# Kernel tuning notes

Measured on AMD Instinct MI355X. Metric: run time of the kernel, lower is better.

## Reference

```python
import jax, jax.numpy as jnp
import numpy as np

# Perfect 8-ary tree, 6 levels, level-order node indexing.
K = 8            # children per internal node
D = 512          # embedding_dim
P = 8            # number of dependency types (num_params)
OFF = [0, 1, 9, 73, 585, 4681, 37449]  # level start offsets; N = 37449
N = OFF[-1]


def setup_inputs() -> dict:
    key = jax.random.key(0)
    ks = jax.random.split(key, 8)
    s = 1.0 / np.sqrt(D)  # torch default-ish init scale, avoids LSTM saturation
    return {
        "embeddings": jax.random.normal(ks[0], (N, D), dtype=jnp.float32),
        "dep_types": jax.random.randint(ks[1], (N,), 0, P, dtype=jnp.int32),
        "W_dep": jax.random.normal(ks[2], (P, D, D), dtype=jnp.float32) * s,
        "b_dep": jax.random.normal(ks[3], (P, D), dtype=jnp.float32) * s,
        "W_ih": jax.random.normal(ks[4], (4 * D, D), dtype=jnp.float32) * s,
        "W_hh": jax.random.normal(ks[5], (4 * D, D), dtype=jnp.float32) * s,
        "b_ih": jax.random.normal(ks[6], (4 * D,), dtype=jnp.float32) * s,
        "b_hh": jax.random.normal(ks[7], (4 * D,), dtype=jnp.float32) * s,
    }


def _lstm_final_c(seq, W_ih, W_hh, b_ih, b_hh):
    # seq: [B, T, D]; 1-layer LSTM with zero init state; returns final cell state c_T [B, D]
    B = seq.shape[0]
    h0 = jnp.zeros((B, D), seq.dtype)

    def step(carry, z_t):
        h, c = carry
        gates = z_t @ W_ih.T + h @ W_hh.T + b_ih + b_hh  # [B, 4D]
        i, f, g, o = jnp.split(gates, 4, axis=-1)        # torch gate order i,f,g,o
        i, f, o = jax.nn.sigmoid(i), jax.nn.sigmoid(f), jax.nn.sigmoid(o)
        g = jnp.tanh(g)
        c = f * c + i * g
        h = o * jnp.tanh(c)
        return (h, c), None

    (h, c), _ = jax.lax.scan(step, (h0, h0), jnp.swapaxes(seq, 0, 1))
    return c


def reference(embeddings, dep_types, W_dep, b_dep, W_ih, W_hh, b_ih, b_hh):
    # Leaves (level 5): LSTM over length-1 sequence [x] -> final cell state.
    leaf_x = embeddings[OFF[5]:OFF[6]]                       # [32768, D]
    z = _lstm_final_c(leaf_x[:, None, :], W_ih, W_hh, b_ih, b_hh)

    # Level-synchronous bottom-up sweep (exactly the recursion's per-node math).
    for l in range(4, -1, -1):
        m = OFF[l + 1] - OFF[l]                              # nodes at this level
        child_z = z.reshape(m, K, D)                         # children's subtree codes
        child_dep = dep_types[OFF[l + 1]:OFF[l + 2]].reshape(m, K)
        onehot = jax.nn.one_hot(child_dep, P, dtype=child_z.dtype)  # [m, K, P]
        # per-dep Linear: z_c = W_dep[dep] @ x_c + b_dep[dep]
        zc = jnp.einsum('mkj,pij,mkp->mki', child_z, W_dep, onehot) + onehot @ b_dep
        x = embeddings[OFF[l]:OFF[l + 1]]                    # node's own embedding, last in seq
        seq = jnp.concatenate([zc, x[:, None, :]], axis=1)   # [m, K+1, D]
        z = _lstm_final_c(seq, W_ih, W_hh, b_ih, b_hh)

    return z  # root sentence embedding, [1, D]
```

## Files before the change

kernel.cpp:

```cpp
#include <hip/hip_runtime.h>

typedef __attribute__((ext_vector_type(8))) short short8;
typedef __attribute__((ext_vector_type(4))) float f32x4;

__device__ __forceinline__ unsigned short f2bf(float x){
  union { float f; unsigned u; } v; v.f = x;
  unsigned r = v.u + 0x7fffu + ((v.u >> 16) & 1u);
  return (unsigned short)(r >> 16);
}
__device__ __forceinline__ float sigm(float x){ return 1.0f / (1.0f + __expf(-x)); }
__device__ __forceinline__ float tanh_(float x){
  float e = __expf(2.0f * x);
  return 1.0f - 2.0f / (e + 1.0f);
}
__device__ __forceinline__ short8 load_bf8_f32(const float* p){
  float4 a = *(const float4*)p;
  float4 b = *(const float4*)(p + 4);
  short8 r;
  r[0]=(short)f2bf(a.x); r[1]=(short)f2bf(a.y); r[2]=(short)f2bf(a.z); r[3]=(short)f2bf(a.w);
  r[4]=(short)f2bf(b.x); r[5]=(short)f2bf(b.y); r[6]=(short)f2bf(b.z); r[7]=(short)f2bf(b.w);
  return r;
}
__device__ __forceinline__ f32x4 mfma16(short8 a, short8 b, f32x4 c){
  return __builtin_amdgcn_mfma_f32_16x16x32_bf16(a, b, c, 0, 0, 0);
}
__device__ __forceinline__ void gload16(const void* g, void* lds){
  __builtin_amdgcn_global_load_lds((const __attribute__((address_space(1))) void*)g,
                                   (__attribute__((address_space(3))) void*)lds, 16, 0, 0);
}
__device__ __forceinline__ f32x4 shfl_xor4(f32x4 v, int m){
  f32x4 r;
  r[0]=__shfl_xor(v[0],m); r[1]=__shfl_xor(v[1],m);
  r[2]=__shfl_xor(v[2],m); r[3]=__shfl_xor(v[3],m);
  return r;
}
__device__ __forceinline__ float pick4(f32x4 v, int k){
  float a = (k&1)? v[1] : v[0];
  float b = (k&1)? v[3] : v[2];
  return (k&2)? b : a;
}
__device__ __forceinline__ f32x4 sel4(f32x4 a0, f32x4 a1, f32x4 a2, f32x4 a3, int k){
  f32x4 x = (k&1)? a1 : a0;
  f32x4 y = (k&1)? a3 : a2;
  return (k&2)? y : x;
}

__global__ __launch_bounds__(256) void conv_plain(const float* __restrict__ in,
                                                  unsigned short* __restrict__ out, int n8){
  for (int i = blockIdx.x*256 + threadIdx.x; i < n8; i += gridDim.x*256)
    *(short8*)(out + (size_t)i*8) = load_bf8_f32(in + (size_t)i*8);
}

__global__ __launch_bounds__(256) void remap4(const float* __restrict__ src,
                                              unsigned short* __restrict__ dst){
  int idx = blockIdx.x*256 + threadIdx.x;
  int r = idx >> 6, c8 = idx & 63;
  int sr = (r & 3)*512 + (r >> 2);
  *(short8*)(dst + (size_t)r*512 + c8*8) = load_bf8_f32(src + (size_t)sr*512 + c8*8);
}
__global__ __launch_bounds__(256) void remap2(const float* __restrict__ src,
                                              unsigned short* __restrict__ dst){
  int idx = blockIdx.x*256 + threadIdx.x;
  int r = idx >> 6, c8 = idx & 63;
  int sr = ((r & 1) ? 2 : 0)*512 + (r >> 1);
  *(short8*)(dst + (size_t)r*512 + c8*8) = load_bf8_f32(src + (size_t)sr*512 + c8*8);
}

__global__ __launch_bounds__(256) void tr_wdep(const float* __restrict__ Wdep,
                                               unsigned short* __restrict__ WdT){
  __shared__ unsigned short tle[64][65];
  int bid = blockIdx.x; int p = bid >> 6; int tile = bid & 63;
  int i0 = (tile >> 3)*64, j0 = (tile & 7)*64;
  const float* src = Wdep + (size_t)p*512*512;
  for (int q = 0; q < 16; ++q){
    int e = q*256 + threadIdx.x;
    int li = e >> 6, lj = e & 63;
    tle[li][lj] = f2bf(src[(size_t)(i0+li)*512 + (j0+lj)]);
  }
  __syncthreads();
  unsigned short* dst = WdT + (size_t)p*512*512;
  for (int q = 0; q < 16; ++q){
    int e = q*256 + threadIdx.x;
    int lj = e >> 6, li = e & 63;
    dst[(size_t)(j0+lj)*512 + (i0+li)] = tle[li][lj];
  }
}

__global__ __launch_bounds__(256) void bsum_k(const float* __restrict__ b_ih,
                                              const float* __restrict__ b_hh,
                                              float* __restrict__ bsum){
  int r = blockIdx.x*256 + threadIdx.x;
  if (r < 2048){ int g = r & 3, j = r >> 2; bsum[r] = b_ih[g*512+j] + b_hh[g*512+j]; }
}
__global__ __launch_bounds__(256) void bc_k(const float* __restrict__ W_ih,
                                            const float* __restrict__ b_dep,
                                            float* __restrict__ bc){
  __shared__ float bd[512];
  int p = blockIdx.x >> 3, ch = blockIdx.x & 7;
  for (int i = threadIdx.x; i < 512; i += 256) bd[i] = b_dep[p*512 + i];
  __syncthreads();
  int r = ch*256 + threadIdx.x;
  int g = r & 3, j = r >> 2;
  const float* wr = W_ih + (size_t)(g*512 + j)*512;
  float s = 0.0f;
  for (int i = 0; i < 512; ++i) s = fmaf(wr[i], bd[i], s);
  bc[(size_t)p*2048 + r] = s;
}

__global__ __launch_bounds__(256) void sort_all(const int* __restrict__ dep,
                                                int* __restrict__ perm,
                                                int* __restrict__ tile_p,
                                                int* __restrict__ meta){
  const int l = blockIdx.x >> 3, t = blockIdx.x & 7;
  const int M_[5]  = {1,8,64,512,4096};
  const int CB_[5] = {1,9,73,585,4681};
  const int MT_[5] = {8,8,8,12,40};
  const int PB_[5] = {69632,61440,53248,40960,0};
  const int TB_[5] = {544,480,416,320,0};
  const int m = M_[l], cb = CB_[l], MT = MT_[l];
  int* pm = perm + PB_[l] + t*MT*128;
  int* tp = tile_p + TB_[l] + t*MT;
  __shared__ int cnt[8], base[8], fill[8];
  if (threadIdx.x < 8){ cnt[threadIdx.x] = 0; fill[threadIdx.x] = 0; }
  __syncthreads();
  for (int n = threadIdx.x; n < m; n += 256) atomicAdd(&cnt[dep[cb + n*8 + t]], 1);
  __syncthreads();
  if (threadIdx.x == 0){
    int tiles = 0;
    for (int p = 0; p < 8; ++p){
      base[p] = tiles*128;
      int g = (cnt[p] + 127) >> 7;
      for (int q = 0; q < g; ++q) tp[tiles + q] = p;
      tiles += g;
    }
    meta[l*8 + t] = tiles;
  }
  __syncthreads();
  for (int i = threadIdx.x; i < MT*128; i += 256) pm[i] = -1;
  __syncthreads();
  for (int n = threadIdx.x; n < m; n += 256){
    int p = dep[cb + n*8 + t];
    pm[base[p] + atomicAdd(&fill[p], 1)] = n;
  }
}

#define KLOOP_BODY(ABASE, BBASE)                                                     \
  for (int kt = 0; kt < 8; ++kt){                                                    \
    _Pragma("unroll")                                                                \
    for (int q = 0; q < 4; ++q){                                                     \
      gload16(ABASE[q] + kt*64, &As[(q*32 + w*8)*64]);                               \
      gload16(BBASE[q] + kt*64, &Bs[(q*32 + w*8)*64]);                               \
    }                                                                                \
    __syncthreads();                                                                 \
    _Pragma("unroll")                                                                \
    for (int kk = 0; kk < 2; ++kk){                                                  \
      short8 av[4], bv[4];                                                           \
      _Pragma("unroll")                                                              \
      for (int i = 0; i < 4; ++i) av[i] = *(const short8*)&As[(wm*64 + i*16 + r15)*64 + kk*32 + g4*8]; \
      _Pragma("unroll")                                                              \
      for (int i = 0; i < 4; ++i) bv[i] = *(const short8*)&Bs[(wn*64 + i*16 + r15)*64 + kk*32 + g4*8]; \
      _Pragma("unroll")                                                              \
      for (int i = 0; i < 4; ++i)                                                    \
        _Pragma("unroll")                                                            \
        for (int j = 0; j < 4; ++j) acc[i][j] = mfma16(av[i], bv[j], acc[i][j]);     \
    }                                                                                \
    __syncthreads();                                                                 \
  }

__global__ __launch_bounds__(256) void combo_gemm(
    const unsigned short* __restrict__ A,
    const unsigned short* __restrict__ WdT,
    unsigned short* __restrict__ C)
{
  const int p  = blockIdx.x >> 6;
  const int mt = (blockIdx.x >> 2) & 15;
  const int nb = blockIdx.x & 3;
  __shared__ unsigned short As[128*64];
  __shared__ unsigned short Bs[128*64];
  const int tid = threadIdx.x, lane = tid & 63, w = tid >> 6;
  const int wm = w >> 1, wn = w & 1;
  const int r15 = lane & 15, g4 = lane >> 4;
  const int kc = (lane & 7)*8;

  const unsigned short* ab[4]; const unsigned short* bb[4];
  #pragma unroll
  for (int q = 0; q < 4; ++q){
    int rl = mt*128 + q*32 + w*8 + (lane >> 3);
    ab[q] = A + (size_t)rl*512 + kc;
    int br = nb*128 + q*32 + w*8 + (lane >> 3);
    bb[q] = WdT + (size_t)p*512*512 + (size_t)br*512 + kc;
  }
  f32x4 acc[4][4] = {};
  KLOOP_BODY(ab, bb)
  unsigned short* Cp = C + (size_t)p*2048*512;
  #pragma unroll
  for (int mi = 0; mi < 4; ++mi)
    #pragma unroll
    for (int ni = 0; ni < 4; ++ni)
      #pragma unroll
      for (int j = 0; j < 4; ++j){
        int row = mt*128 + wm*64 + mi*16 + g4*4 + j;
        int col = nb*128 + wn*64 + ni*16 + r15;
        Cp[(size_t)row*512 + col] = f2bf(acc[mi][ni][j]);
      }
}

__global__ __launch_bounds__(256) void leaf_gemm(
    const unsigned short* __restrict__ embL,
    const unsigned short* __restrict__ Wleaf,
    const float* __restrict__ bsum,
    unsigned short* __restrict__ zo)
{
  const int nb = blockIdx.x & 7;
  const int mt = blockIdx.x >> 3;
  __shared__ unsigned short As[128*64];
  __shared__ unsigned short Bs[128*64];
  const int tid = threadIdx.x, lane = tid & 63, w = tid >> 6;
  const int wm = w >> 1, wn = w & 1;
  const int r15 = lane & 15, g4 = lane >> 4;
  const int kc = (lane & 7)*8;

  const unsigned short* ab[4]; const unsigned short* bb[4];
  #pragma unroll
  for (int q = 0; q < 4; ++q){
    int rl = mt*128 + q*32 + w*8 + (lane >> 3);
    ab[q] = embL + (size_t)rl*512 + kc;
    int br = nb*128 + q*32 + w*8 + (lane >> 3);
    bb[q] = Wleaf + (size_t)br*512 + kc;
  }
  f32x4 acc[4][4] = {};
  KLOOP_BODY(ab, bb)
  const int g2 = r15 & 1;
  #pragma unroll
  for (int ni = 0; ni < 4; ++ni){
    int ci = nb*128 + wn*64 + ni*16 + r15;
    float b = bsum[4*(ci >> 1) + (g2 ? 2 : 0)];
    #pragma unroll
    for (int mi = 0; mi < 4; ++mi){
      acc[mi][ni][0]+=b; acc[mi][ni][1]+=b; acc[mi][ni][2]+=b; acc[mi][ni][3]+=b;
    }
  }
  #pragma unroll
  for (int mi = 0; mi < 4; ++mi)
    #pragma unroll
    for (int ni = 0; ni < 4; ++ni){
      f32x4 a0 = acc[mi][ni];
      f32x4 a1 = shfl_xor4(a0, 1);
      f32x4 vi_ = g2 ? a1 : a0;
      f32x4 vg_ = g2 ? a0 : a1;
      int jz = (nb*128 + wn*64 + ni*16 + r15) >> 1;
      #pragma unroll
      for (int u = 0; u < 2; ++u){
        int jrow = (g2 << 1) + u;
        float zi = pick4(vi_, jrow), zg = pick4(vg_, jrow);
        int row = mt*128 + wm*64 + mi*16 + g4*4 + jrow;
        zo[(size_t)row*512 + jz] = f2bf(sigm(zi) * tanh_(zg));
      }
    }
}

__global__ __launch_bounds__(256) void step_kernel(
    const unsigned short* __restrict__ zin,
    const unsigned short* __restrict__ embL,
    const unsigned short* __restrict__ Bx,
    const unsigned short* __restrict__ Whh,
    const int* __restrict__ perm,
    const int* __restrict__ tile_p,
    const int* __restrict__ meta,
    const float* __restrict__ bsum,
    const float* __restrict__ bcomb,
    const unsigned short* __restrict__ hin,
    unsigned short* __restrict__ hout,
    float* __restrict__ cbuf,
    unsigned short* __restrict__ zout,
    float* __restrict__ fout,
    int m, int t, int first, int last)
{
  const int nb = blockIdx.x & 15;
  const int mt = blockIdx.x >> 4;
  if (meta && mt >= *meta) return;
  const int p = tile_p ? tile_p[mt] : 0;

  __shared__ unsigned short As[128*64];
  __shared__ unsigned short Bs[128*64];
  const int tid = threadIdx.x, lane = tid & 63, w = tid >> 6;
  const int wm = w >> 1, wn = w & 1;
  const int r15 = lane & 15, g4 = lane >> 4;
  const int kc = (lane & 7)*8;

  int nn[4];
  #pragma unroll
  for (int q = 0; q < 4; ++q){
    int rl = mt*128 + q*32 + w*8 + (lane >> 3);
    int n = perm ? perm[rl] : (rl < m ? rl : 0);
    nn[q] = (n < 0) ? 0 : n;
  }
  const unsigned short* BxP = Bx + (size_t)p*2048*512;

  f32x4 acc[4][4] = {};
  {
    const unsigned short* ab[4]; const unsigned short* bb[4];
    #pragma unroll
    for (int q = 0; q < 4; ++q){
      ab[q] = perm ? (zin + ((size_t)nn[q]*8 + t)*512 + kc)
                   : (embL + (size_t)nn[q]*512 + kc);
      int br = nb*128 + q*32 + w*8 + (lane >> 3);
      bb[q] = BxP + (size_t)br*512 + kc;
    }
    KLOOP_BODY(ab, bb)
  }
  if (!first){
    const unsigned short* ab[4]; const unsigned short* bb[4];
    #pragma unroll
    for (int q = 0; q < 4; ++q){
      ab[q] = hin + (size_t)nn[q]*512 + kc;
      int br = nb*128 + q*32 + w*8 + (lane >> 3);
      bb[q] = Whh + (size_t)br*512 + kc;
    }
    KLOOP_BODY(ab, bb)
  }

  const int gate = r15 & 3;
  #pragma unroll
  for (int ni = 0; ni < 4; ++ni){
    int ci = nb*128 + wn*64 + ni*16 + r15;
    float b = bsum[ci] + (bcomb ? bcomb[(size_t)p*2048 + ci] : 0.0f);
    #pragma unroll
    for (int mi = 0; mi < 4; ++mi){
      acc[mi][ni][0]+=b; acc[mi][ni][1]+=b; acc[mi][ni][2]+=b; acc[mi][ni][3]+=b;
    }
  }
  const int jr = r15 & 3;
  #pragma unroll
  for (int mi = 0; mi < 4; ++mi){
    int rl = mt*128 + wm*64 + mi*16 + g4*4 + jr;
    int n = perm ? perm[rl] : (rl < m ? rl : -1);
    #pragma unroll
    for (int ni = 0; ni < 4; ++ni){
      f32x4 a0 = acc[mi][ni];
      f32x4 a1 = shfl_xor4(a0, 1);
      f32x4 a2 = shfl_xor4(a0, 2);
      f32x4 a3 = shfl_xor4(a1, 2);
      f32x4 vi_ = sel4(a0,a1,a2,a3, gate);
      f32x4 vf_ = sel4(a0,a1,a2,a3, gate^1);
      f32x4 vg_ = sel4(a0,a1,a2,a3, gate^2);
      f32x4 vo_ = sel4(a0,a1,a2,a3, gate^3);
      float xi = pick4(vi_, jr), xf = pick4(vf_, jr);
      float xg = pick4(vg_, jr), xo = pick4(vo_, jr);
      if (n >= 0){
        int jz = nb*32 + wn*16 + ni*4 + (r15 >> 2);
        size_t idx = (size_t)n*512 + jz;
        float i_ = sigm(xi), f_ = sigm(xf), g_ = tanh_(xg), o_ = sigm(xo);
        float cold = first ? 0.0f : cbuf[idx];
        float cn = fmaf(f_, cold, i_*g_);
        if (!last){ cbuf[idx] = cn; hout[idx] = f2bf(o_*tanh_(cn)); }
        else { if (zout) zout[idx] = f2bf(cn); if (fout) fout[idx] = cn; }
      }
    }
  }
}

extern "C" void kernel_launch(void* const* d_in, const int* in_sizes, int n_in,
                              void* d_out, int out_size, void* d_ws, size_t ws_size,
                              hipStream_t stream)
{
  (void)in_sizes; (void)n_in; (void)out_size; (void)ws_size;
  const float* emb   = (const float*)d_in[0];
  const int*   dep   = (const int*)  d_in[1];
  const float* W_dep = (const float*)d_in[2];
  const float* b_dep = (const float*)d_in[3];
  const float* W_ih  = (const float*)d_in[4];
  const float* W_hh  = (const float*)d_in[5];
  const float* b_ih  = (const float*)d_in[6];
  const float* b_hh  = (const float*)d_in[7];
  float* out = (float*)d_out;

  unsigned short* embb   = (unsigned short*)d_ws;
  unsigned short* Wih_il = embb   + 19173888ull;
  unsigned short* Whh_il = Wih_il + 1048576ull;
  unsigned short* Wleaf  = Whh_il + 1048576ull;
  unsigned short* WdT    = Wleaf  + 524288ull;
  unsigned short* Wcombo = WdT    + 2097152ull;
  unsigned short* Z0     = Wcombo + 8388608ull;
  unsigned short* Z1     = Z0     + 16777216ull;
  unsigned short* hA     = Z1     + 2097152ull;
  unsigned short* hB     = hA     + 2097152ull;
  float* cbuf  = (float*)(hB + 2097152ull);
  float* bsum  = cbuf + 2097152ull;
  float* bc    = bsum + 2048;
  int*  perm   = (int*)(bc + 16384);
  int*  tile_p = perm + 77824;
  int*  meta   = tile_p + 608;

  conv_plain<<<2048, 256, 0, stream>>>(emb, embb, 2396736);
  remap4<<<512, 256, 0, stream>>>(W_ih, Wih_il);
  remap4<<<512, 256, 0, stream>>>(W_hh, Whh_il);
  remap2<<<256, 256, 0, stream>>>(W_ih, Wleaf);
  tr_wdep<<<512, 256, 0, stream>>>(W_dep, WdT);
  bsum_k<<<8, 256, 0, stream>>>(b_ih, b_hh, bsum);
  bc_k<<<64, 256, 0, stream>>>(W_ih, b_dep, bc);
  combo_gemm<<<512, 256, 0, stream>>>(Wih_il, WdT, Wcombo);
  sort_all<<<40, 256, 0, stream>>>(dep, perm, tile_p, meta);
  leaf_gemm<<<2048, 256, 0, stream>>>(embb + (size_t)4681*512, Wleaf, bsum, Z0);

  const int LM[5]  = {1, 8, 64, 512, 4096};
  const int LNB[5] = {0, 1, 9, 73, 585};
  const int LMT[5] = {8, 8, 8, 12, 40};
  const int LPB[5] = {69632, 61440, 53248, 40960, 0};
  const int LTB[5] = {544, 480, 416, 320, 0};

  int zi_idx = 0;
  unsigned short* zbufs[2] = {Z0, Z1};
  for (int l = 4; l >= 0; --l){
    unsigned short* zin = zbufs[zi_idx];
    unsigned short* zo  = zbufs[zi_idx ^ 1];
    int m = LM[l];
    for (int t = 0; t <= 8; ++t){
      int first = (t == 0), last = (t == 8);
      unsigned short* hi = (t & 1) ? hA : hB;
      unsigned short* ho = (t & 1) ? hB : hA;
      int grid = (t < 8) ? LMT[l]*16 : ((m + 127)/128)*16;
      step_kernel<<<grid, 256, 0, stream>>>(
          zin, embb + (size_t)LNB[l]*512,
          (t < 8) ? Wcombo : Wih_il, Whh_il,
          (t < 8) ? (perm + LPB[l] + t*LMT[l]*128) : nullptr,
          (t < 8) ? (tile_p + LTB[l] + t*LMT[l]) : nullptr,
          (t < 8) ? (meta + l*8 + t) : nullptr,
          bsum, (t < 8) ? bc : nullptr,
          hi, ho, cbuf,
          (last && l > 0) ? zo : nullptr,
          (last && l == 0) ? out : nullptr,
          m, t, first, last);
    }
    zi_idx ^= 1;
  }
}
```

Measured before the change: 1.515 ms.

## Fuse prep kernels and run tree sweep as one cooperative persistent kernel

Merges the preprocessing kernels (conversions, transposes, bias sums, sorting) into a single multi-role prep kernel. The combo GEMM, leaf GEMM and all 45 level/timestep steps become phases of one cooperative persistent kernel with grid-wide syncs between them, removing many kernel launches and their gaps. It falls back to per-phase launches if the cooperative launch fails. The trade-offs are grid-sync overhead, a grid capped at 640 blocks that must loop over jobs in the large phases, and possible register or occupancy pressure from the merged kernel.

```diff
diff --git a/kernel.cpp b/kernel.cpp
--- a/kernel.cpp
+++ b/kernel.cpp
@@ -1,4 +1,7 @@
 #include <hip/hip_runtime.h>
+#include <hip/hip_cooperative_groups.h>
+
+namespace cg = cooperative_groups;
 
 typedef __attribute__((ext_vector_type(8))) short short8;
 typedef __attribute__((ext_vector_type(4))) float f32x4;
@@ -43,105 +46,6 @@
   f32x4 x = (k&1)? a1 : a0;
   f32x4 y = (k&1)? a3 : a2;
   return (k&2)? y : x;
-}
-
-__global__ __launch_bounds__(256) void conv_plain(const float* __restrict__ in,
-                                                  unsigned short* __restrict__ out, int n8){
-  for (int i = blockIdx.x*256 + threadIdx.x; i < n8; i += gridDim.x*256)
-    *(short8*)(out + (size_t)i*8) = load_bf8_f32(in + (size_t)i*8);
-}
-
-__global__ __launch_bounds__(256) void remap4(const float* __restrict__ src,
-                                              unsigned short* __restrict__ dst){
-  int idx = blockIdx.x*256 + threadIdx.x;
-  int r = idx >> 6, c8 = idx & 63;
-  int sr = (r & 3)*512 + (r >> 2);
-  *(short8*)(dst + (size_t)r*512 + c8*8) = load_bf8_f32(src + (size_t)sr*512 + c8*8);
-}
-__global__ __launch_bounds__(256) void remap2(const float* __restrict__ src,
-                                              unsigned short* __restrict__ dst){
-  int idx = blockIdx.x*256 + threadIdx.x;
-  int r = idx >> 6, c8 = idx & 63;
-  int sr = ((r & 1) ? 2 : 0)*512 + (r >> 1);
-  *(short8*)(dst + (size_t)r*512 + c8*8) = load_bf8_f32(src + (size_t)sr*512 + c8*8);
-}
-
-__global__ __launch_bounds__(256) void tr_wdep(const float* __restrict__ Wdep,
-                                               unsigned short* __restrict__ WdT){
-  __shared__ unsigned short tle[64][65];
-  int bid = blockIdx.x; int p = bid >> 6; int tile = bid & 63;
-  int i0 = (tile >> 3)*64, j0 = (tile & 7)*64;
-  const float* src = Wdep + (size_t)p*512*512;
-  for (int q = 0; q < 16; ++q){
-    int e = q*256 + threadIdx.x;
-    int li = e >> 6, lj = e & 63;
-    tle[li][lj] = f2bf(src[(size_t)(i0+li)*512 + (j0+lj)]);
-  }
-  __syncthreads();
-  unsigned short* dst = WdT + (size_t)p*512*512;
-  for (int q = 0; q < 16; ++q){
-    int e = q*256 + threadIdx.x;
-    int lj = e >> 6, li = e & 63;
-    dst[(size_t)(j0+lj)*512 + (i0+li)] = tle[li][lj];
-  }
-}
-
-__global__ __launch_bounds__(256) void bsum_k(const float* __restrict__ b_ih,
-                                              const float* __restrict__ b_hh,
-                                              float* __restrict__ bsum){
-  int r = blockIdx.x*256 + threadIdx.x;
-  if (r < 2048){ int g = r & 3, j = r >> 2; bsum[r] = b_ih[g*512+j] + b_hh[g*512+j]; }
-}
-__global__ __launch_bounds__(256) void bc_k(const float* __restrict__ W_ih,
-                                            const float* __restrict__ b_dep,
-                                            float* __restrict__ bc){
-  __shared__ float bd[512];
-  int p = blockIdx.x >> 3, ch = blockIdx.x & 7;
-  for (int i = threadIdx.x; i < 512; i += 256) bd[i] = b_dep[p*512 + i];
-  __syncthreads();
-  int r = ch*256 + threadIdx.x;
-  int g = r & 3, j = r >> 2;
-  const float* wr = W_ih + (size_t)(g*512 + j)*512;
-  float s = 0.0f;
-  for (int i = 0; i < 512; ++i) s = fmaf(wr[i], bd[i], s);
-  bc[(size_t)p*2048 + r] = s;
-}
-
-__global__ __launch_bounds__(256) void sort_all(const int* __restrict__ dep,
-                                                int* __restrict__ perm,
-                                                int* __restrict__ tile_p,
-                                                int* __restrict__ meta){
-  const int l = blockIdx.x >> 3, t = blockIdx.x & 7;
-  const int M_[5]  = {1,8,64,512,4096};
-  const int CB_[5] = {1,9,73,585,4681};
-  const int MT_[5] = {8,8,8,12,40};
-  const int PB_[5] = {69632,61440,53248,40960,0};
-  const int TB_[5] = {544,480,416,320,0};
-  const int m = M_[l], cb = CB_[l], MT = MT_[l];
-  int* pm = perm + PB_[l] + t*MT*128;
-  int* tp = tile_p + TB_[l] + t*MT;
-  __shared__ int cnt[8], base[8], fill[8];
-  if (threadIdx.x < 8){ cnt[threadIdx.x] = 0; fill[threadIdx.x] = 0; }
-  __syncthreads();
-  for (int n = threadIdx.x; n < m; n += 256) atomicAdd(&cnt[dep[cb + n*8 + t]], 1);
-  __syncthreads();
-  if (threadIdx.x == 0){
-    int tiles = 0;
-    for (int p = 0; p < 8; ++p){
-      base[p] = tiles*128;
-      int g = (cnt[p] + 127) >> 7;
-      for (int q = 0; q < g; ++q) tp[tiles + q] = p;
-      tiles += g;
-    }
-    meta[l*8 + t] = tiles;
-  }
-  __syncthreads();
-  for (int i = threadIdx.x; i < MT*128; i += 256) pm[i] = -1;
-  __syncthreads();
-  for (int n = threadIdx.x; n < m; n += 256){
-    int p = dep[cb + n*8 + t];
-    pm[base[p] + atomicAdd(&fill[p], 1)] = n;
-  }
 }
 
 #define KLOOP_BODY(ABASE, BBASE)                                                     \
@@ -167,196 +71,297 @@
     __syncthreads();                                                                 \
   }
 
-__global__ __launch_bounds__(256) void combo_gemm(
-    const unsigned short* __restrict__ A,
-    const unsigned short* __restrict__ WdT,
-    unsigned short* __restrict__ C)
+__global__ __launch_bounds__(256) void prep_kernel(
+    const float* __restrict__ emb, const int* __restrict__ dep,
+    const float* __restrict__ W_dep, const float* __restrict__ b_dep,
+    const float* __restrict__ W_ih, const float* __restrict__ W_hh,
+    const float* __restrict__ b_ih, const float* __restrict__ b_hh,
+    unsigned short* __restrict__ embb, unsigned short* __restrict__ Wih_il,
+    unsigned short* __restrict__ Whh_il, unsigned short* __restrict__ Wleaf,
+    unsigned short* __restrict__ WdT, float* __restrict__ bsum, float* __restrict__ bc,
+    int* __restrict__ perm, int* __restrict__ tile_p, int* __restrict__ meta)
 {
-  const int p  = blockIdx.x >> 6;
-  const int mt = (blockIdx.x >> 2) & 15;
-  const int nb = blockIdx.x & 3;
+  const int bid = blockIdx.x, tid = threadIdx.x;
+  if (bid < 1024){
+    for (size_t i = (size_t)bid*256 + tid; i < 2396736ull; i += 1024ull*256)
+      *(short8*)(embb + i*8) = load_bf8_f32(emb + i*8);
+  } else if (bid < 1536){
+    int idx = (bid-1024)*256 + tid; int r = idx >> 6, c8 = idx & 63;
+    int sr = (r & 3)*512 + (r >> 2);
+    *(short8*)(Wih_il + (size_t)r*512 + c8*8) = load_bf8_f32(W_ih + (size_t)sr*512 + c8*8);
+  } else if (bid < 2048){
+    int idx = (bid-1536)*256 + tid; int r = idx >> 6, c8 = idx & 63;
+    int sr = (r & 3)*512 + (r >> 2);
+    *(short8*)(Whh_il + (size_t)r*512 + c8*8) = load_bf8_f32(W_hh + (size_t)sr*512 + c8*8);
+  } else if (bid < 2304){
+    int idx = (bid-2048)*256 + tid; int r = idx >> 6, c8 = idx & 63;
+    int sr = ((r & 1) ? 2 : 0)*512 + (r >> 1);
+    *(short8*)(Wleaf + (size_t)r*512 + c8*8) = load_bf8_f32(W_ih + (size_t)sr*512 + c8*8);
+  } else if (bid < 2816){
+    __shared__ unsigned short tle[64][65];
+    int lb = bid - 2304; int p = lb >> 6; int tile = lb & 63;
+    int i0 = (tile >> 3)*64, j0 = (tile & 7)*64;
+    const float* src = W_dep + (size_t)p*512*512;
+    for (int q = 0; q < 16; ++q){
+      int e = q*256 + tid; int li = e >> 6, lj = e & 63;
+      tle[li][lj] = f2bf(src[(size_t)(i0+li)*512 + (j0+lj)]);
+    }
+    __syncthreads();
+    unsigned short* dst = WdT + (size_t)p*512*512;
+    for (int q = 0; q < 16; ++q){
+      int e = q*256 + tid; int lj = e >> 6, li = e & 63;
+      dst[(size_t)(j0+lj)*512 + (i0+li)] = tle[li][lj];
+    }
+  } else if (bid < 2824){
+    int r = (bid-2816)*256 + tid;
+    if (r < 2048){ int g = r & 3, j = r >> 2; bsum[r] = b_ih[g*512+j] + b_hh[g*512+j]; }
+  } else if (bid < 2888){
+    __shared__ float bd[512];
+    int lb = bid - 2824; int p = lb >> 3, ch = lb & 7;
+    for (int i = tid; i < 512; i += 256) bd[i] = b_dep[p*512 + i];
+    __syncthreads();
+    int r = ch*256 + tid; int g = r & 3, j = r >> 2;
+    const float* wr = W_ih + (size_t)(g*512 + j)*512;
+    float s = 0.0f;
+    for (int i = 0; i < 512; ++i) s = fmaf(wr[i], bd[i], s);
+    bc[(size_t)p*2048 + r] = s;
+  } else {
+    __shared__ int cnt[8], base[8], fill[8];
+    int lb = bid - 2888; const int l = lb >> 3, t = lb & 7;
+    const int M_[5]  = {1,8,64,512,4096};
+    const int CB_[5] = {1,9,73,585,4681};
+    const int MT_[5] = {8,8,8,12,40};
+    const int PB_[5] = {69632,61440,53248,40960,0};
+    const int TB_[5] = {544,480,416,320,0};
+    const int m = M_[l], cb = CB_[l], MT = MT_[l];
+    int* pm = perm + PB_[l] + t*MT*128;
+    int* tp = tile_p + TB_[l] + t*MT;
+    if (tid < 8){ cnt[tid] = 0; fill[tid] = 0; }
+    __syncthreads();
+    for (int n = tid; n < m; n += 256) atomicAdd(&cnt[dep[cb + n*8 + t]], 1);
+    __syncthreads();
+    if (tid == 0){
+      int tiles = 0;
+      for (int p = 0; p < 8; ++p){
+        base[p] = tiles*128;
+        int g = (cnt[p] + 127) >> 7;
+        for (int q = 0; q < g; ++q) tp[tiles + q] = p;
+        tiles += g;
+      }
+      meta[l*8 + t] = tiles;
+    }
+    __syncthreads();
+    for (int i = tid; i < MT*128; i += 256) pm[i] = -1;
+    __syncthreads();
+    for (int n = tid; n < m; n += 256){
+      int p = dep[cb + n*8 + t];
+      pm[base[p] + atomicAdd(&fill[p], 1)] = n;
+    }
+  }
+}
+
+struct TreeArgs {
+  const unsigned short* embb;
+  const unsigned short* Wih_il;
+  const unsigned short* Whh_il;
+  const unsigned short* Wleaf;
+  const unsigned short* WdT;
+  unsigned short* Wcombo;
+  unsigned short* Z0;
+  unsigned short* Z1;
+  unsigned short* hA;
+  unsigned short* hB;
+  float* cbuf;
+  const float* bsum;
+  const float* bc;
+  const int* perm;
+  const int* tile_p;
+  const int* meta;
+  float* out;
+};
+
+__global__ __launch_bounds__(256, 2) void tree_kernel(TreeArgs a, int phase_lo, int phase_hi)
+{
+  cg::grid_group gg = cg::this_grid();
   __shared__ unsigned short As[128*64];
   __shared__ unsigned short Bs[128*64];
   const int tid = threadIdx.x, lane = tid & 63, w = tid >> 6;
   const int wm = w >> 1, wn = w & 1;
   const int r15 = lane & 15, g4 = lane >> 4;
   const int kc = (lane & 7)*8;
-
-  const unsigned short* ab[4]; const unsigned short* bb[4];
-  #pragma unroll
-  for (int q = 0; q < 4; ++q){
-    int rl = mt*128 + q*32 + w*8 + (lane >> 3);
-    ab[q] = A + (size_t)rl*512 + kc;
-    int br = nb*128 + q*32 + w*8 + (lane >> 3);
-    bb[q] = WdT + (size_t)p*512*512 + (size_t)br*512 + kc;
-  }
-  f32x4 acc[4][4] = {};
-  KLOOP_BODY(ab, bb)
-  unsigned short* Cp = C + (size_t)p*2048*512;
-  #pragma unroll
-  for (int mi = 0; mi < 4; ++mi)
-    #pragma unroll
-    for (int ni = 0; ni < 4; ++ni)
-      #pragma unroll
-      for (int j = 0; j < 4; ++j){
-        int row = mt*128 + wm*64 + mi*16 + g4*4 + j;
-        int col = nb*128 + wn*64 + ni*16 + r15;
-        Cp[(size_t)row*512 + col] = f2bf(acc[mi][ni][j]);
+  const int GS = gridDim.x;
+
+  for (int ph = phase_lo; ph <= phase_hi; ++ph){
+    if (ph == 0){
+      for (int job = blockIdx.x; job < 2560; job += GS){
+        if (job < 512){
+          const int p = job >> 6, mt = (job >> 2) & 15, nbq = job & 3;
+          const unsigned short* ab[4]; const unsigned short* bb[4];
+          #pragma unroll
+          for (int q = 0; q < 4; ++q){
+            int rl = mt*128 + q*32 + w*8 + (lane >> 3);
+            ab[q] = a.Wih_il + (size_t)rl*512 + kc;
+            int br = nbq*128 + q*32 + w*8 + (lane >> 3);
+            bb[q] = a.WdT + (size_t)p*262144 + (size_t)br*512 + kc;
+          }
+          f32x4 acc[4][4] = {};
+          KLOOP_BODY(ab, bb)
+          unsigned short* Cp = a.Wcombo + (size_t)p*1048576;
+          #pragma unroll
+          for (int mi = 0; mi < 4; ++mi)
+            #pragma unroll
+            for (int ni = 0; ni < 4; ++ni)
+              #pragma unroll
+              for (int j = 0; j < 4; ++j){
+                int row = mt*128 + wm*64 + mi*16 + g4*4 + j;
+                int col = nbq*128 + wn*64 + ni*16 + r15;
+                Cp[(size_t)row*512 + col] = f2bf(acc[mi][ni][j]);
+              }
+        } else {
+          const int lj = job - 512;
+          const int mt = lj >> 3, nbq = lj & 7;
+          const unsigned short* ab[4]; const unsigned short* bb[4];
+          #pragma unroll
+          for (int q = 0; q < 4; ++q){
+            int rl = mt*128 + q*32 + w*8 + (lane >> 3);
+            ab[q] = a.embb + (size_t)(4681 + rl)*512 + kc;
+            int br = nbq*128 + q*32 + w*8 + (lane >> 3);
+            bb[q] = a.Wleaf + (size_t)br*512 + kc;
+          }
+          f32x4 acc[4][4] = {};
+          KLOOP_BODY(ab, bb)
+          const int g2 = r15 & 1;
+          #pragma unroll
+          for (int ni = 0; ni < 4; ++ni){
+            int ci = nbq*128 + wn*64 + ni*16 + r15;
+            float b = a.bsum[4*(ci >> 1) + (g2 ? 2 : 0)];
+            #pragma unroll
+            for (int mi = 0; mi < 4; ++mi){
+              acc[mi][ni][0]+=b; acc[mi][ni][1]+=b; acc[mi][ni][2]+=b; acc[mi][ni][3]+=b;
+            }
+          }
+          #pragma unroll
+          for (int mi = 0; mi < 4; ++mi)
+            #pragma unroll
+            for (int ni = 0; ni < 4; ++ni){
+              f32x4 a0 = acc[mi][ni];
+              f32x4 a1 = shfl_xor4(a0, 1);
+              f32x4 vi_ = g2 ? a1 : a0;
+              f32x4 vg_ = g2 ? a0 : a1;
+              int jz = (nbq*128 + wn*64 + ni*16 + r15) >> 1;
+              #pragma unroll
+              for (int u = 0; u < 2; ++u){
+                int jrow = (g2 << 1) + u;
+                float zi = pick4(vi_, jrow), zg = pick4(vg_, jrow);
+                int row = mt*128 + wm*64 + mi*16 + g4*4 + jrow;
+                a.Z0[(size_t)row*512 + jz] = f2bf(sigm(zi) * tanh_(zg));
+              }
+            }
+        }
       }
-}
-
-__global__ __launch_bounds__(256) void leaf_gemm(
-    const unsigned short* __restrict__ embL,
-    const unsigned short* __restrict__ Wleaf,
-    const float* __restrict__ bsum,
-    unsigned short* __restrict__ zo)
-{
-  const int nb = blockIdx.x & 7;
-  const int mt = blockIdx.x >> 3;
-  __shared__ unsigned short As[128*64];
-  __shared__ unsigned short Bs[128*64];
-  const int tid = threadIdx.x, lane = tid & 63, w = tid >> 6;
-  const int wm = w >> 1, wn = w & 1;
-  const int r15 = lane & 15, g4 = lane >> 4;
-  const int kc = (lane & 7)*8;
-
-  const unsigned short* ab[4]; const unsigned short* bb[4];
-  #pragma unroll
-  for (int q = 0; q < 4; ++q){
-    int rl = mt*128 + q*32 + w*8 + (lane >> 3);
-    ab[q] = embL + (size_t)rl*512 + kc;
-    int br = nb*128 + q*32 + w*8 + (lane >> 3);
-    bb[q] = Wleaf + (size_t)br*512 + kc;
-  }
-  f32x4 acc[4][4] = {};
-  KLOOP_BODY(ab, bb)
-  const int g2 = r15 & 1;
-  #pragma unroll
-  for (int ni = 0; ni < 4; ++ni){
-    int ci = nb*128 + wn*64 + ni*16 + r15;
-    float b = bsum[4*(ci >> 1) + (g2 ? 2 : 0)];
-    #pragma unroll
-    for (int mi = 0; mi < 4; ++mi){
-      acc[mi][ni][0]+=b; acc[mi][ni][1]+=b; acc[mi][ni][2]+=b; acc[mi][ni][3]+=b;
-    }
-  }
-  #pragma unroll
-  for (int mi = 0; mi < 4; ++mi)
-    #pragma unroll
-    for (int ni = 0; ni < 4; ++ni){
-      f32x4 a0 = acc[mi][ni];
-      f32x4 a1 = shfl_xor4(a0, 1);
-      f32x4 vi_ = g2 ? a1 : a0;
-      f32x4 vg_ = g2 ? a0 : a1;
-      int jz = (nb*128 + wn*64 + ni*16 + r15) >> 1;
-      #pragma unroll
-      for (int u = 0; u < 2; ++u){
-        int jrow = (g2 << 1) + u;
-        float zi = pick4(vi_, jrow), zg = pick4(vg_, jrow);
-        int row = mt*128 + wm*64 + mi*16 + g4*4 + jrow;
-        zo[(size_t)row*512 + jz] = f2bf(sigm(zi) * tanh_(zg));
+    } else {
+      const int s = ph - 1;
+      const int dl = s / 9;
+      const int l = 4 - dl;
+      const int t = s - dl*9;
+      const int m = 1 << (3*l);
+      const int node_base = (m - 1) / 7;
+      int MT, PB, TB;
+      if (l == 4)      { MT = 40; PB = 0;     TB = 0;   }
+      else if (l == 3) { MT = 12; PB = 40960; TB = 320; }
+      else if (l == 2) { MT = 8;  PB = 53248; TB = 416; }
+      else if (l == 1) { MT = 8;  PB = 61440; TB = 480; }
+      else             { MT = 8;  PB = 69632; TB = 544; }
+      const unsigned short* zin = (l & 1) ? a.Z1 : a.Z0;
+      unsigned short* zo        = (l & 1) ? a.Z0 : a.Z1;
+      const int first = (t == 0), last = (t == 8);
+      const unsigned short* hi = (t & 1) ? a.hA : a.hB;
+      unsigned short* ho       = (t & 1) ? a.hB : a.hA;
+
+      int njobs; const int* pm = nullptr; const int* tp = nullptr;
+      if (t < 8){
+        int ntiles = a.meta[l*8 + t]; if (ntiles > MT) ntiles = MT;
+        njobs = ntiles * 16;
+        pm = a.perm + PB + t*MT*128;
+        tp = a.tile_p + TB + t*MT;
+      } else {
+        njobs = ((m + 127) >> 7) * 16;
       }
-    }
-}
-
-__global__ __launch_bounds__(256) void step_kernel(
-    const unsigned short* __restrict__ zin,
-    const unsigned short* __restrict__ embL,
-    const unsigned short* __restrict__ Bx,
-    const unsigned short* __restrict__ Whh,
-    const int* __restrict__ perm,
-    const int* __restrict__ tile_p,
-    const int* __restrict__ meta,
-    const float* __restrict__ bsum,
-    const float* __restrict__ bcomb,
-    const unsigned short* __restrict__ hin,
-    unsigned short* __restrict__ hout,
-    float* __restrict__ cbuf,
-    unsigned short* __restrict__ zout,
-    float* __restrict__ fout,
-    int m, int t, int first, int last)
-{
-  const int nb = blockIdx.x & 15;
-  const int mt = blockIdx.x >> 4;
-  if (meta && mt >= *meta) return;
-  const int p = tile_p ? tile_p[mt] : 0;
-
-  __shared__ unsigned short As[128*64];
-  __shared__ unsigned short Bs[128*64];
-  const int tid = threadIdx.x, lane = tid & 63, w = tid >> 6;
-  const int wm = w >> 1, wn = w & 1;
-  const int r15 = lane & 15, g4 = lane >> 4;
-  const int kc = (lane & 7)*8;
-
-  int nn[4];
-  #pragma unroll
-  for (int q = 0; q < 4; ++q){
-    int rl = mt*128 + q*32 + w*8 + (lane >> 3);
-    int n = perm ? perm[rl] : (rl < m ? rl : 0);
-    nn[q] = (n < 0) ? 0 : n;
-  }
-  const unsigned short* BxP = Bx + (size_t)p*2048*512;
-
-  f32x4 acc[4][4] = {};
-  {
-    const unsigned short* ab[4]; const unsigned short* bb[4];
-    #pragma unroll
-    for (int q = 0; q < 4; ++q){
-      ab[q] = perm ? (zin + ((size_t)nn[q]*8 + t)*512 + kc)
-                   : (embL + (size_t)nn[q]*512 + kc);
-      int br = nb*128 + q*32 + w*8 + (lane >> 3);
-      bb[q] = BxP + (size_t)br*512 + kc;
-    }
-    KLOOP_BODY(ab, bb)
-  }
-  if (!first){
-    const unsigned short* ab[4]; const unsigned short* bb[4];
-    #pragma unroll
-    for (int q = 0; q < 4; ++q){
-      ab[q] = hin + (size_t)nn[q]*512 + kc;
-      int br = nb*128 + q*32 + w*8 + (lane >> 3);
-      bb[q] = Whh + (size_t)br*512 + kc;
-    }
-    KLOOP_BODY(ab, bb)
-  }
-
-  const int gate = r15 & 3;
-  #pragma unroll
-  for (int ni = 0; ni < 4; ++ni){
-    int ci = nb*128 + wn*64 + ni*16 + r15;
-    float b = bsum[ci] + (bcomb ? bcomb[(size_t)p*2048 + ci] : 0.0f);
-    #pragma unroll
-    for (int mi = 0; mi < 4; ++mi){
-      acc[mi][ni][0]+=b; acc[mi][ni][1]+=b; acc[mi][ni][2]+=b; acc[mi][ni][3]+=b;
-    }
-  }
-  const int jr = r15 & 3;
-  #pragma unroll
-  for (int mi = 0; mi < 4; ++mi){
-    int rl = mt*128 + wm*64 + mi*16 + g4*4 + jr;
-    int n = perm ? perm[rl] : (rl < m ? rl : -1);
-    #pragma unroll
-    for (int ni = 0; ni < 4; ++ni){
-      f32x4 a0 = acc[mi][ni];
-      f32x4 a1 = shfl_xor4(a0, 1);
-      f32x4 a2 = shfl_xor4(a0, 2);
-      f32x4 a3 = shfl_xor4(a1, 2);
-      f32x4 vi_ = sel4(a0,a1,a2,a3, gate);
-      f32x4 vf_ = sel4(a0,a1,a2,a3, gate^1);
-      f32x4 vg_ = sel4(a0,a1,a2,a3, gate^2);
-      f32x4 vo_ = sel4(a0,a1,a2,a3, gate^3);
-      float xi = pick4(vi_, jr), xf = pick4(vf_, jr);
-      float xg = pick4(vg_, jr), xo = pick4(vo_, jr);
-      if (n >= 0){
-        int jz = nb*32 + wn*16 + ni*4 + (r15 >> 2);
-        size_t idx = (size_t)n*512 + jz;
-        float i_ = sigm(xi), f_ = sigm(xf), g_ = tanh_(xg), o_ = sigm(xo);
-        float cold = first ? 0.0f : cbuf[idx];
-        float cn = fmaf(f_, cold, i_*g_);
-        if (!last){ cbuf[idx] = cn; hout[idx] = f2bf(o_*tanh_(cn)); }
-        else { if (zout) zout[idx] = f2bf(cn); if (fout) fout[idx] = cn; }
+
+      for (int job = blockIdx.x; job < njobs; job += GS){
+        const int mt = job >> 4, nbq = job & 15;
+        const int p = (t < 8) ? tp[mt] : 0;
+        int nn[4];
+        #pragma unroll
+        for (int q = 0; q < 4; ++q){
+          int rl = mt*128 + q*32 + w*8 + (lane >> 3);
+          int n = (t < 8) ? pm[rl] : (rl < m ? rl : -1);
+          nn[q] = (n < 0) ? 0 : n;
+        }
+        f32x4 acc[4][4] = {};
+        {
+          const unsigned short* Bx = (t < 8) ? (a.Wcombo + (size_t)p*1048576) : a.Wih_il;
+          const unsigned short* ab[4]; const unsigned short* bb[4];
+          #pragma unroll
+          for (int q = 0; q < 4; ++q){
+            ab[q] = (t < 8) ? (zin + ((size_t)nn[q]*8 + t)*512 + kc)
+                            : (a.embb + (size_t)(node_base + nn[q])*512 + kc);
+            int br = nbq*128 + q*32 + w*8 + (lane >> 3);
+            bb[q] = Bx + (size_t)br*512 + kc;
+          }
+          KLOOP_BODY(ab, bb)
+        }
+        if (!first){
+          const unsigned short* ab[4]; const unsigned short* bb[4];
+          #pragma unroll
+          for (int q = 0; q < 4; ++q){
+            ab[q] = hi + (size_t)nn[q]*512 + kc;
+            int br = nbq*128 + q*32 + w*8 + (lane >> 3);
+            bb[q] = a.Whh_il + (size_t)br*512 + kc;
+          }
+          KLOOP_BODY(ab, bb)
+        }
+        const int gate = r15 & 3;
+        #pragma unroll
+        for (int ni = 0; ni < 4; ++ni){
+          int ci = nbq*128 + wn*64 + ni*16 + r15;
+          float b = a.bsum[ci] + ((t < 8) ? a.bc[(size_t)p*2048 + ci] : 0.0f);
+          #pragma unroll
+          for (int mi = 0; mi < 4; ++mi){
+            acc[mi][ni][0]+=b; acc[mi][ni][1]+=b; acc[mi][ni][2]+=b; acc[mi][ni][3]+=b;
+          }
+        }
+        const int jr = r15 & 3;
+        #pragma unroll
+        for (int mi = 0; mi < 4; ++mi){
+          int rl = mt*128 + wm*64 + mi*16 + g4*4 + jr;
+          int n = (t < 8) ? pm[rl] : (rl < m ? rl : -1);
+          #pragma unroll
+          for (int ni = 0; ni < 4; ++ni){
+            f32x4 a0 = acc[mi][ni];
+            f32x4 a1 = shfl_xor4(a0, 1);
+            f32x4 a2 = shfl_xor4(a0, 2);
+            f32x4 a3 = shfl_xor4(a1, 2);
+            f32x4 vi_ = sel4(a0,a1,a2,a3, gate);
+            f32x4 vf_ = sel4(a0,a1,a2,a3, gate^1);
+            f32x4 vg_ = sel4(a0,a1,a2,a3, gate^2);
+            f32x4 vo_ = sel4(a0,a1,a2,a3, gate^3);
+            float xi = pick4(vi_, jr), xf = pick4(vf_, jr);
+            float xg = pick4(vg_, jr), xo = pick4(vo_, jr);
+            if (n >= 0){
+              int jz = nbq*32 + wn*16 + ni*4 + (r15 >> 2);
+              size_t idx = (size_t)n*512 + jz;
+              float i_ = sigm(xi), f_ = sigm(xf), g_ = tanh_(xg), o_ = sigm(xo);
+              float cold = first ? 0.0f : a.cbuf[idx];
+              float cn = fmaf(f_, cold, i_*g_);
+              if (!last){ a.cbuf[idx] = cn; ho[idx] = f2bf(o_*tanh_(cn)); }
+              else { if (l > 0) zo[idx] = f2bf(cn); else a.out[idx] = cn; }
+            }
+          }
+        }
       }
     }
+    if (ph != phase_hi) gg.sync();
   }
 }
 
@@ -392,46 +397,42 @@
   int*  tile_p = perm + 77824;
   int*  meta   = tile_p + 608;
 
-  conv_plain<<<2048, 256, 0, stream>>>(emb, embb, 2396736);
-  remap4<<<512, 256, 0, stream>>>(W_ih, Wih_il);
-  remap4<<<512, 256, 0, stream>>>(W_hh, Whh_il);
-  remap2<<<256, 256, 0, stream>>>(W_ih, Wleaf);
-  tr_wdep<<<512, 256, 0, stream>>>(W_dep, WdT);
-  bsum_k<<<8, 256, 0, stream>>>(b_ih, b_hh, bsum);
-  bc_k<<<64, 256, 0, stream>>>(W_ih, b_dep, bc);
-  combo_gemm<<<512, 256, 0, stream>>>(Wih_il, WdT, Wcombo);
-  sort_all<<<40, 256, 0, stream>>>(dep, perm, tile_p, meta);
-  leaf_gemm<<<2048, 256, 0, stream>>>(embb + (size_t)4681*512, Wleaf, bsum, Z0);
-
-  const int LM[5]  = {1, 8, 64, 512, 4096};
-  const int LNB[5] = {0, 1, 9, 73, 585};
-  const int LMT[5] = {8, 8, 8, 12, 40};
-  const int LPB[5] = {69632, 61440, 53248, 40960, 0};
-  const int LTB[5] = {544, 480, 416, 320, 0};
-
-  int zi_idx = 0;
-  unsigned short* zbufs[2] = {Z0, Z1};
-  for (int l = 4; l >= 0; --l){
-    unsigned short* zin = zbufs[zi_idx];
-    unsigned short* zo  = zbufs[zi_idx ^ 1];
-    int m = LM[l];
-    for (int t = 0; t <= 8; ++t){
-      int first = (t == 0), last = (t == 8);
-      unsigned short* hi = (t & 1) ? hA : hB;
-      unsigned short* ho = (t & 1) ? hB : hA;
-      int grid = (t < 8) ? LMT[l]*16 : ((m + 127)/128)*16;
-      step_kernel<<<grid, 256, 0, stream>>>(
-          zin, embb + (size_t)LNB[l]*512,
-          (t < 8) ? Wcombo : Wih_il, Whh_il,
-          (t < 8) ? (perm + LPB[l] + t*LMT[l]*128) : nullptr,
-          (t < 8) ? (tile_p + LTB[l] + t*LMT[l]) : nullptr,
-          (t < 8) ? (meta + l*8 + t) : nullptr,
-          bsum, (t < 8) ? bc : nullptr,
-          hi, ho, cbuf,
-          (last && l > 0) ? zo : nullptr,
-          (last && l == 0) ? out : nullptr,
-          m, t, first, last);
-    }
-    zi_idx ^= 1;
+  prep_kernel<<<2928, 256, 0, stream>>>(emb, dep, W_dep, b_dep, W_ih, W_hh, b_ih, b_hh,
+                                        embb, Wih_il, Whh_il, Wleaf, WdT, bsum, bc,
+                                        perm, tile_p, meta);
+
+  TreeArgs ta;
+  ta.embb = embb; ta.Wih_il = Wih_il; ta.Whh_il = Whh_il; ta.Wleaf = Wleaf;
+  ta.WdT = WdT; ta.Wcombo = Wcombo; ta.Z0 = Z0; ta.Z1 = Z1; ta.hA = hA; ta.hB = hB;
+  ta.cbuf = cbuf; ta.bsum = bsum; ta.bc = bc; ta.perm = perm; ta.tile_p = tile_p;
+  ta.meta = meta; ta.out = out;
+
+  int cap = 0, nCU = 0, dev = 0;
+  (void)hipGetDevice(&dev);
+  (void)hipOccupancyMaxActiveBlocksPerMultiprocessor(&cap, tree_kernel, 256, 0);
+  (void)hipDeviceGetAttribute(&nCU, hipDeviceAttributeMultiprocessorCount, dev);
+  if (nCU <= 0) nCU = 256;
+  long capacity = (long)cap * nCU;
+  int gsz = (int)((capacity < 640) ? capacity : 640);
+
+  hipError_t ce = hipErrorUnknown;
+  if (gsz >= 64){
+    int plo = 0, phi = 45;
+    void* kp[3] = { &ta, &plo, &phi };
+    ce = hipLaunchCooperativeKernel((const void*)tree_kernel, dim3(gsz), dim3(256),
+                                    kp, 0, stream);
   }
-}
+  if (ce != hipSuccess){
+    for (int ph = 0; ph <= 45; ++ph){
+      int grid;
+      if (ph == 0) grid = 2560;
+      else {
+        int s = ph - 1, dl = s/9, l = 4 - dl, t = s - dl*9;
+        int m = 1 << (3*l);
+        int MT = (l == 4) ? 40 : (l == 3) ? 12 : 8;
+        grid = (t < 8) ? MT*16 : ((m + 127) >> 7)*16;
+      }
+      tree_kernel<<<grid, 256, 0, stream>>>(ta, ph, ph);
+    }
+  }
+}
```

Result: slower. 2.788 ms (+84.0%).
